# Performance work log

Measured on AMD Instinct MI355X. Metric: run time of the kernel, lower is better.

## Reference

```python
import jax, jax.numpy as jnp
import numpy as np

# Graph sizes: each graph has exactly 32 nodes (forced by the rearrange + lin1 in_features)
BS = 4096
NODES = 32
N = BS * NODES          # 131072 total nodes
F_IN = 128
E_PER_G = 512
E = BS * E_PER_G        # 2097152 edges, all within-graph
HID = 1024
NCLS = 10


def setup_inputs() -> dict:
    key = jax.random.key(0)
    ks = jax.random.split(key, 9)
    x = jax.random.normal(ks[0], (N, F_IN), dtype=jnp.float32)
    # within-graph random edges: local node ids in [0,32) + per-graph offset
    graph_off = jnp.repeat(jnp.arange(BS, dtype=jnp.int64), E_PER_G) * NODES
    src = jax.random.randint(ks[1], (E,), 0, NODES, dtype=jnp.int64) + graph_off
    dst = jax.random.randint(ks[2], (E,), 0, NODES, dtype=jnp.int64) + graph_off
    edge_index = jnp.stack([src, dst], axis=0)
    s = 0.05
    gconv_w = jax.random.normal(ks[3], (F_IN, F_IN), dtype=jnp.float32) * s
    gconv_b = jax.random.normal(ks[4], (F_IN,), dtype=jnp.float32) * s
    lin1_w = jax.random.normal(ks[5], (HID, F_IN * NODES), dtype=jnp.float32) * s
    lin1_b = jax.random.normal(ks[6], (HID,), dtype=jnp.float32) * s
    lin2_w = jax.random.normal(ks[7], (NCLS, HID), dtype=jnp.float32) * s
    lin2_b = jax.random.normal(ks[8], (NCLS,), dtype=jnp.float32) * s
    return {"x": x, "edge_index": edge_index, "gconv_w": gconv_w,
            "gconv_b": gconv_b, "lin1_w": lin1_w, "lin1_b": lin1_b,
            "lin2_w": lin2_w, "lin2_b": lin2_b, "bs": BS}


def reference(x, edge_index, gconv_w, gconv_b, lin1_w, lin1_b, lin2_w, lin2_b, bs):
    # GINConv (eps=0): h_i = Linear( x_i + sum_{j->i} x_j )
    src, dst = edge_index[0], edge_index[1]
    agg = jax.ops.segment_sum(x[src], dst, num_segments=x.shape[0])  # [N, F]
    h = (x + agg) @ gconv_w.T + gconv_b                               # [N, F]
    h = jax.nn.relu(h)
    # rearrange '(bs e) f -> bs (f e)' with e=32 nodes per graph
    f = h.shape[-1]
    h = h.reshape(bs, NODES, f).transpose(0, 2, 1).reshape(bs, f * NODES)
    h = h @ lin1_w.T + lin1_b
    # dropout is identity in eval mode
    h = jax.nn.relu(h)
    h = h @ lin2_w.T + lin2_b
    return jax.nn.softmax(h, axis=-1)
```

## Files before the change

kernel.cpp:

```cpp
#include <hip/hip_runtime.h>

typedef _Float16 half_t;
typedef _Float16 halfv8 __attribute__((ext_vector_type(8)));
typedef _Float16 halfv4 __attribute__((ext_vector_type(4)));
typedef float    floatv4 __attribute__((ext_vector_type(4)));
typedef unsigned int uint;
typedef uint uintv4 __attribute__((ext_vector_type(4)));

#define NODES 32
#define FIN   128
#define EPG   512
#define NBS   4096
#define ETOT  (NBS*EPG)
#define HID   1024
#define KDIM  4096
#define NCLS  10
#define WPITCH 136
#define YPITCH 36

#define GLDS16(g, l)                                                        \
  __builtin_amdgcn_global_load_lds(                                         \
      (const __attribute__((address_space(1))) unsigned int*)(g),           \
      (__attribute__((address_space(3))) unsigned int*)(l), 16, 0, 0)

__global__ __launch_bounds__(256) void prep_w1(const float* __restrict__ w1,
                                               half_t* __restrict__ w1p) {
  __shared__ float tmp[FIN * 33];
  const int o = blockIdx.x, t = threadIdx.x;
  const floatv4* src = (const floatv4*)(w1 + (size_t)o * KDIM);
  for (int i = t; i < KDIM / 4; i += 256) {
    floatv4 v = src[i];
    const int f = i >> 3;
    const int n = (i & 7) * 4;
#pragma unroll
    for (int q = 0; q < 4; ++q) tmp[f * 33 + n + q] = v[q];
  }
  __syncthreads();
  half_t* dst = w1p + (size_t)o * KDIM;
  for (int i = t; i < KDIM; i += 256) {
    const int n = i >> 7, f = i & 127;
    dst[i] = (half_t)tmp[f * 33 + n];
  }
}

__global__ __launch_bounds__(256, 2) void gin_fused(
    const float* __restrict__ x, const int* __restrict__ ei,
    const float* __restrict__ gw, const float* __restrict__ gb,
    half_t* __restrict__ H) {
  __shared__ __attribute__((aligned(16))) half_t Ws[FIN * WPITCH];
  __shared__ __attribute__((aligned(16))) half_t Yt[4][FIN * YPITCH];
  __shared__ __attribute__((aligned(16))) uint  cnt[4][512];

  const int t = threadIdx.x, w = t >> 6, l = t & 63;
  const int lr = l & 15, lk = l >> 4;
  const int g = blockIdx.x * 4 + w;

  const float* xg = x + (size_t)g * (NODES * FIN);
  floatv4 xr[2][4][2];
#pragma unroll
  for (int mt = 0; mt < 2; ++mt)
#pragma unroll
    for (int kk = 0; kk < 4; ++kk) {
      const float* p = xg + (mt * 16 + lr) * FIN + kk * 32 + lk * 8;
      xr[mt][kk][0] = *(const floatv4*)p;
      xr[mt][kk][1] = *(const floatv4*)(p + 4);
    }
  const int* sp = ei + (size_t)g * EPG;
  const int* dp = ei + (size_t)ETOT + (size_t)g * EPG;
  uintv4 s0 = *(const uintv4*)(sp + l * 8);
  uintv4 s1 = *(const uintv4*)(sp + l * 8 + 4);
  uintv4 d0 = *(const uintv4*)(dp + l * 8);
  uintv4 d1 = *(const uintv4*)(dp + l * 8 + 4);

  {
    uintv4* c4 = (uintv4*)cnt[w];
    uintv4 z = {0, 0, 0, 0};
    c4[l] = z;
    c4[l + 64] = z;
  }
  for (int i = t; i < (FIN * FIN) / 4; i += 256) {
    const int o = i >> 5, kc = (i & 31) * 4;
    floatv4 v = *(const floatv4*)(gw + o * FIN + kc);
    halfv4 h = {(half_t)v[0], (half_t)v[1], (half_t)v[2], (half_t)v[3]};
    *(halfv4*)&Ws[o * WPITCH + kc] = h;
  }
  __syncthreads();

#pragma unroll
  for (int q = 0; q < 4; ++q) {
    uint p0 = (d0[q] & 31) * 32 + (s0[q] & 31);
    atomicAdd(&cnt[w][p0 >> 1], 1u << ((p0 & 1) * 16));
    uint p1 = (d1[q] & 31) * 32 + (s1[q] & 31);
    atomicAdd(&cnt[w][p1 >> 1], 1u << ((p1 & 1) * 16));
  }

  halfv8 af[2][4];
#pragma unroll
  for (int mt = 0; mt < 2; ++mt)
#pragma unroll
    for (int kk = 0; kk < 4; ++kk) {
      halfv8 h;
#pragma unroll
      for (int q = 0; q < 4; ++q) {
        h[q]     = (half_t)xr[mt][kk][0][q];
        h[q + 4] = (half_t)xr[mt][kk][1][q];
      }
      af[mt][kk] = h;
    }

  floatv4 acc[2][8] = {};
#pragma unroll
  for (int kk = 0; kk < 4; ++kk)
#pragma unroll
    for (int nt = 0; nt < 8; ++nt) {
      halfv8 bf = *(const halfv8*)&Ws[(nt * 16 + lr) * WPITCH + kk * 32 + lk * 8];
#pragma unroll
      for (int mt = 0; mt < 2; ++mt)
        acc[mt][nt] = __builtin_amdgcn_mfma_f32_16x16x32_f16(af[mt][kk], bf,
                                                             acc[mt][nt], 0, 0, 0);
    }

  half_t* yw = Yt[w];
#pragma unroll
  for (int mt = 0; mt < 2; ++mt)
#pragma unroll
    for (int nt = 0; nt < 8; ++nt) {
      halfv4 h = {(half_t)acc[mt][nt][0], (half_t)acc[mt][nt][1],
                  (half_t)acc[mt][nt][2], (half_t)acc[mt][nt][3]};
      *(halfv4*)&yw[(nt * 16 + lr) * YPITCH + mt * 16 + lk * 4] = h;
    }

  const unsigned short* c16 = (const unsigned short*)cnt[w];
  halfv8 am[2];
#pragma unroll
  for (int mt = 0; mt < 2; ++mt) {
    const int i = mt * 16 + lr;
#pragma unroll
    for (int q = 0; q < 8; ++q) {
      const int j = lk * 8 + q;
      float c = (float)c16[i * 32 + j] + ((j == i) ? 1.f : 0.f);
      am[mt][q] = (half_t)c;
    }
  }

  floatv4 acc2[2][8] = {};
#pragma unroll
  for (int nt = 0; nt < 8; ++nt) {
    halfv8 bf = *(const halfv8*)&yw[(nt * 16 + lr) * YPITCH + lk * 8];
#pragma unroll
    for (int mt = 0; mt < 2; ++mt)
      acc2[mt][nt] = __builtin_amdgcn_mfma_f32_16x16x32_f16(am[mt], bf,
                                                            acc2[mt][nt], 0, 0, 0);
  }

  half_t* Hg = H + (size_t)g * KDIM;
#pragma unroll
  for (int nt = 0; nt < 8; ++nt) {
    const float bias = gb[nt * 16 + lr];
#pragma unroll
    for (int mt = 0; mt < 2; ++mt)
#pragma unroll
      for (int q = 0; q < 4; ++q) {
        const int m = mt * 16 + lk * 4 + q;
        const float v = acc2[mt][nt][q] + bias;
        Hg[m * FIN + nt * 16 + lr] = (half_t)(v > 0.f ? v : 0.f);
      }
  }
}

__global__ __launch_bounds__(256) void lin1_gemm(
    const half_t* __restrict__ A, const half_t* __restrict__ B,
    half_t* __restrict__ Cbase) {
  __shared__ __attribute__((aligned(16))) half_t As[128 * 32];
  __shared__ __attribute__((aligned(16))) half_t Bs[128 * 32];
  const int t = threadIdx.x;
  const int m0 = blockIdx.x * 128;
  const int n0 = blockIdx.y * 128;
  const int kz = blockIdx.z;
  const int k0 = kz * (KDIM / 2);
  half_t* C = Cbase + (size_t)kz * ((size_t)NBS * HID);

  const int w = t >> 6, l = t & 63;
  const int lr = l & 15, lk = l >> 4;
  const int wm = (w & 1) * 64, wn = (w >> 1) * 64;

  const int ch0 = t, ch1 = t + 256;
  const int r0 = ch0 >> 2, c0_ = (ch0 & 3) * 8;
  const int r1 = ch1 >> 2, c1_ = (ch1 & 3) * 8;
  const half_t* gA0 = A + (size_t)(m0 + r0) * KDIM + k0 + c0_;
  const half_t* gA1 = A + (size_t)(m0 + r1) * KDIM + k0 + c1_;
  const half_t* gB0 = B + (size_t)(n0 + r0) * KDIM + k0 + c0_;
  const half_t* gB1 = B + (size_t)(n0 + r1) * KDIM + k0 + c1_;

  floatv4 acc[4][4] = {};

  for (int kt = 0; kt < 64; ++kt) {
    GLDS16(gA0, &As[ch0 * 8]);
    GLDS16(gA1, &As[ch1 * 8]);
    GLDS16(gB0, &Bs[ch0 * 8]);
    GLDS16(gB1, &Bs[ch1 * 8]);
    gA0 += 32; gA1 += 32; gB0 += 32; gB1 += 32;
    __syncthreads();

    halfv8 af[4], bf[4];
#pragma unroll
    for (int mf = 0; mf < 4; ++mf)
      af[mf] = *(const halfv8*)&As[(wm + mf * 16 + lr) * 32 + lk * 8];
#pragma unroll
    for (int nf = 0; nf < 4; ++nf)
      bf[nf] = *(const halfv8*)&Bs[(wn + nf * 16 + lr) * 32 + lk * 8];
#pragma unroll
    for (int mf = 0; mf < 4; ++mf)
#pragma unroll
      for (int nf = 0; nf < 4; ++nf)
        acc[mf][nf] = __builtin_amdgcn_mfma_f32_16x16x32_f16(af[mf], bf[nf],
                                                             acc[mf][nf], 0, 0, 0);
    __syncthreads();
  }
#pragma unroll
  for (int mf = 0; mf < 4; ++mf)
#pragma unroll
    for (int nf = 0; nf < 4; ++nf) {
      const int n = n0 + wn + nf * 16 + lr;
#pragma unroll
      for (int j = 0; j < 4; ++j) {
        const int m = m0 + wm + mf * 16 + lk * 4 + j;
        C[(size_t)m * HID + n] = (half_t)acc[mf][nf][j];
      }
    }
}

__global__ __launch_bounds__(256) void head(
    const half_t* __restrict__ C0, const half_t* __restrict__ C1,
    const float* __restrict__ b1, const float* __restrict__ w2,
    const float* __restrict__ b2, float* __restrict__ out) {
  __shared__ __attribute__((aligned(16))) float w2s[NCLS * HID];
  const int t = threadIdx.x;
  {
    const floatv4* s4 = (const floatv4*)w2;
    floatv4* d4 = (floatv4*)w2s;
    for (int i = t; i < (NCLS * HID) / 4; i += 256) d4[i] = s4[i];
  }
  __syncthreads();
  const int w = t >> 6, l = t & 63;
  const int row = blockIdx.x * 4 + w;
  const half_t* c0 = C0 + (size_t)row * HID;
  const half_t* c1 = C1 + (size_t)row * HID;

  float r[16];
#pragma unroll
  for (int jj = 0; jj < 4; ++jj) {
    halfv4 u = *(const halfv4*)&c0[jj * 256 + l * 4];
    halfv4 v = *(const halfv4*)&c1[jj * 256 + l * 4];
    floatv4 bb = *(const floatv4*)&b1[jj * 256 + l * 4];
#pragma unroll
    for (int q = 0; q < 4; ++q) {
      const float s = (float)u[q] + (float)v[q] + bb[q];
      r[jj * 4 + q] = s > 0.f ? s : 0.f;
    }
  }
  float lg[10];
#pragma unroll
  for (int c = 0; c < NCLS; ++c) {
    float p = 0.f;
#pragma unroll
    for (int jj = 0; jj < 4; ++jj) {
      floatv4 wv = *(const floatv4*)&w2s[c * HID + jj * 256 + l * 4];
      p += r[jj * 4 + 0] * wv[0] + r[jj * 4 + 1] * wv[1] +
           r[jj * 4 + 2] * wv[2] + r[jj * 4 + 3] * wv[3];
    }
#pragma unroll
    for (int off = 32; off >= 1; off >>= 1) p += __shfl_xor(p, off);
    lg[c] = p + b2[c];
  }
  float mx = lg[0];
#pragma unroll
  for (int c = 1; c < NCLS; ++c) mx = fmaxf(mx, lg[c]);
  float sum = 0.f;
#pragma unroll
  for (int c = 0; c < NCLS; ++c) { lg[c] = __expf(lg[c] - mx); sum += lg[c]; }
  const float inv = 1.f / sum;
  float myv = 0.f;
#pragma unroll
  for (int c = 0; c < NCLS; ++c) myv = (l == c) ? lg[c] * inv : myv;
  if (l < NCLS) out[(size_t)row * NCLS + l] = myv;
}

extern "C" void kernel_launch(void* const* d_in, const int* in_sizes, int n_in,
                              void* d_out, int out_size, void* d_ws, size_t ws_size,
                              hipStream_t stream) {
  (void)in_sizes; (void)n_in; (void)out_size; (void)ws_size;
  const float* x  = (const float*)d_in[0];
  const int*   ei = (const int*)d_in[1];
  const float* gw = (const float*)d_in[2];
  const float* gb = (const float*)d_in[3];
  const float* w1 = (const float*)d_in[4];
  const float* b1 = (const float*)d_in[5];
  const float* w2 = (const float*)d_in[6];
  const float* b2 = (const float*)d_in[7];
  float* out = (float*)d_out;

  char* ws = (char*)d_ws;
  half_t* H   = (half_t*)(ws);
  half_t* w1p = (half_t*)(ws + 33554432);
  half_t* C01 = (half_t*)(ws + 33554432 + 8388608);

  prep_w1  <<<dim3(HID),       dim3(256), 0, stream>>>(w1, w1p);
  gin_fused<<<dim3(NBS / 4),   dim3(256), 0, stream>>>(x, ei, gw, gb, H);
  lin1_gemm<<<dim3(32, 8, 2),  dim3(256), 0, stream>>>(H, w1p, C01);
  head     <<<dim3(NBS / 4),   dim3(256), 0, stream>>>(C01, C01 + (size_t)NBS * HID,
                                                       b1, w2, b2, out);
}
```

Measured before the change: 100.3 us.

## Rewrite lin1 GEMM with 256x256 tiles, double-buffered swizzled LDS, 4-way split-K

Replaces the 128x128x32 single-buffered lin1 GEMM with 512-thread blocks computing 256x256 tiles and BK=64. Global-to-LDS loads are double-buffered, LDS chunks are XOR-swizzled to avoid bank conflicts, and MFMA bursts are bracketed with setprio. The block index is remapped to group tiles, and K is split four ways, so the head kernel now sums four fp16 partials. This aims to cut global traffic per flop and hide load latency. The costs are more partial-sum traffic and LDS pressure: 128KB per block with launch_bounds(512,2).

```diff
diff --git a/kernel.cpp b/kernel.cpp
--- a/kernel.cpp
+++ b/kernel.cpp
@@ -18,6 +18,13 @@
 #define WPITCH 136
 #define YPITCH 36
 
+#define BM 256
+#define BN 256
+#define BK 64
+#define KS 4
+#define KSLEN (KDIM/KS)
+#define NT (KSLEN/BK)
+
 #define GLDS16(g, l)                                                        \
   __builtin_amdgcn_global_load_lds(                                         \
       (const __attribute__((address_space(1))) unsigned int*)(g),           \
@@ -168,72 +175,125 @@
   }
 }
 
-__global__ __launch_bounds__(256) void lin1_gemm(
+__global__ __launch_bounds__(512, 2) void lin1_gemm(
     const half_t* __restrict__ A, const half_t* __restrict__ B,
     half_t* __restrict__ Cbase) {
-  __shared__ __attribute__((aligned(16))) half_t As[128 * 32];
-  __shared__ __attribute__((aligned(16))) half_t Bs[128 * 32];
+  __shared__ __attribute__((aligned(16))) half_t As[2][BM * BK];
+  __shared__ __attribute__((aligned(16))) half_t Bs[2][BN * BK];
+
   const int t = threadIdx.x;
-  const int m0 = blockIdx.x * 128;
-  const int n0 = blockIdx.y * 128;
-  const int kz = blockIdx.z;
-  const int k0 = kz * (KDIM / 2);
-  half_t* C = Cbase + (size_t)kz * ((size_t)NBS * HID);
-
-  const int w = t >> 6, l = t & 63;
-  const int lr = l & 15, lk = l >> 4;
-  const int wm = (w & 1) * 64, wn = (w >> 1) * 64;
-
-  const int ch0 = t, ch1 = t + 256;
-  const int r0 = ch0 >> 2, c0_ = (ch0 & 3) * 8;
-  const int r1 = ch1 >> 2, c1_ = (ch1 & 3) * 8;
-  const half_t* gA0 = A + (size_t)(m0 + r0) * KDIM + k0 + c0_;
-  const half_t* gA1 = A + (size_t)(m0 + r1) * KDIM + k0 + c1_;
-  const half_t* gB0 = B + (size_t)(n0 + r0) * KDIM + k0 + c0_;
-  const half_t* gB1 = B + (size_t)(n0 + r1) * KDIM + k0 + c1_;
-
-  floatv4 acc[4][4] = {};
-
-  for (int kt = 0; kt < 64; ++kt) {
-    GLDS16(gA0, &As[ch0 * 8]);
-    GLDS16(gA1, &As[ch1 * 8]);
-    GLDS16(gB0, &Bs[ch0 * 8]);
-    GLDS16(gB1, &Bs[ch1 * 8]);
-    gA0 += 32; gA1 += 32; gB0 += 32; gB1 += 32;
-    __syncthreads();
-
-    halfv8 af[4], bf[4];
-#pragma unroll
-    for (int mf = 0; mf < 4; ++mf)
-      af[mf] = *(const halfv8*)&As[(wm + mf * 16 + lr) * 32 + lk * 8];
-#pragma unroll
-    for (int nf = 0; nf < 4; ++nf)
-      bf[nf] = *(const halfv8*)&Bs[(wn + nf * 16 + lr) * 32 + lk * 8];
-#pragma unroll
-    for (int mf = 0; mf < 4; ++mf)
-#pragma unroll
-      for (int nf = 0; nf < 4; ++nf)
-        acc[mf][nf] = __builtin_amdgcn_mfma_f32_16x16x32_f16(af[mf], bf[nf],
-                                                             acc[mf][nf], 0, 0, 0);
-    __syncthreads();
-  }
-#pragma unroll
-  for (int mf = 0; mf < 4; ++mf)
+  const int orig = blockIdx.x;
+  const int wg = (orig & 7) * 32 + (orig >> 3);
+  const int mt = wg & 15, rest = wg >> 4;
+  const int nt_ = rest & 3, ks = rest >> 2;
+  const int m0 = mt * BM, n0 = nt_ * BN, k0 = ks * KSLEN;
+
+  const half_t* gA[4];
+  const half_t* gB[4];
+#pragma unroll
+  for (int j = 0; j < 4; ++j) {
+    const int L = t + j * 512;
+    const int r = L >> 3;
+    const int c = (L & 7) ^ (r & 7);
+    gA[j] = A + (size_t)(m0 + r) * KDIM + k0 + c * 8;
+    gB[j] = B + (size_t)(n0 + r) * KDIM + k0 + c * 8;
+  }
+
+#define STAGE(buf, koff)                                                    \
+  {                                                                         \
+    _Pragma("unroll")                                                       \
+    for (int j = 0; j < 4; ++j)                                             \
+      GLDS16(gA[j] + (koff), &As[buf][(t + j * 512) * 8]);                  \
+    _Pragma("unroll")                                                       \
+    for (int j = 0; j < 4; ++j)                                             \
+      GLDS16(gB[j] + (koff), &Bs[buf][(t + j * 512) * 8]);                  \
+  }
+
+  const int w = t >> 6, l = t & 63, lr = l & 15, lk = l >> 4;
+  const int wm = (w >> 2) * 128, wn = (w & 3) * 64;
+
+  floatv4 acc[8][4] = {};
+
+  STAGE(0, 0)
+  STAGE(1, BK)
+  asm volatile("s_waitcnt vmcnt(8)" ::: "memory");
+  __builtin_amdgcn_s_barrier();
+
+  for (int kt = 0; kt < NT; ++kt) {
+    const int cur = kt & 1;
+    const half_t* as = As[cur];
+    const half_t* bs = Bs[cur];
+    halfv8 bf[4], af[4];
+#pragma unroll
+    for (int ksb = 0; ksb < 2; ++ksb) {
+#pragma unroll
+      for (int nf = 0; nf < 4; ++nf) {
+        const int row = wn + nf * 16 + lr;
+        const int ch = (ksb * 4 + lk) ^ (row & 7);
+        bf[nf] = *(const halfv8*)&bs[row * BK + ch * 8];
+      }
+#pragma unroll
+      for (int mf = 0; mf < 4; ++mf) {
+        const int row = wm + mf * 16 + lr;
+        const int ch = (ksb * 4 + lk) ^ (row & 7);
+        af[mf] = *(const halfv8*)&as[row * BK + ch * 8];
+      }
+      __builtin_amdgcn_s_barrier();
+      asm volatile("s_waitcnt lgkmcnt(0)" ::: "memory");
+      __builtin_amdgcn_sched_barrier(0);
+      __builtin_amdgcn_s_setprio(1);
+#pragma unroll
+      for (int mf = 0; mf < 4; ++mf)
+#pragma unroll
+        for (int nf = 0; nf < 4; ++nf)
+          acc[mf][nf] = __builtin_amdgcn_mfma_f32_16x16x32_f16(
+              af[mf], bf[nf], acc[mf][nf], 0, 0, 0);
+      __builtin_amdgcn_s_setprio(0);
+      __builtin_amdgcn_s_barrier();
+#pragma unroll
+      for (int mf = 0; mf < 4; ++mf) {
+        const int row = wm + 64 + mf * 16 + lr;
+        const int ch = (ksb * 4 + lk) ^ (row & 7);
+        af[mf] = *(const halfv8*)&as[row * BK + ch * 8];
+      }
+      __builtin_amdgcn_s_barrier();
+      asm volatile("s_waitcnt lgkmcnt(0)" ::: "memory");
+      __builtin_amdgcn_sched_barrier(0);
+      __builtin_amdgcn_s_setprio(1);
+#pragma unroll
+      for (int mf = 0; mf < 4; ++mf)
+#pragma unroll
+        for (int nf = 0; nf < 4; ++nf)
+          acc[mf + 4][nf] = __builtin_amdgcn_mfma_f32_16x16x32_f16(
+              af[mf], bf[nf], acc[mf + 4][nf], 0, 0, 0);
+      __builtin_amdgcn_s_setprio(0);
+      __builtin_amdgcn_s_barrier();
+    }
+    const int src = (kt + 2 < NT) ? (kt + 2) : 0;
+    STAGE(cur, src * BK)
+    asm volatile("s_waitcnt vmcnt(8)" ::: "memory");
+    __builtin_amdgcn_s_barrier();
+  }
+
+  half_t* C = Cbase + (size_t)ks * ((size_t)NBS * HID);
+#pragma unroll
+  for (int mf = 0; mf < 8; ++mf)
 #pragma unroll
     for (int nf = 0; nf < 4; ++nf) {
       const int n = n0 + wn + nf * 16 + lr;
 #pragma unroll
-      for (int j = 0; j < 4; ++j) {
-        const int m = m0 + wm + mf * 16 + lk * 4 + j;
-        C[(size_t)m * HID + n] = (half_t)acc[mf][nf][j];
-      }
-    }
+      for (int q = 0; q < 4; ++q) {
+        const int m = m0 + wm + mf * 16 + lk * 4 + q;
+        C[(size_t)m * HID + n] = (half_t)acc[mf][nf][q];
+      }
+    }
+#undef STAGE
 }
 
 __global__ __launch_bounds__(256) void head(
-    const half_t* __restrict__ C0, const half_t* __restrict__ C1,
-    const float* __restrict__ b1, const float* __restrict__ w2,
-    const float* __restrict__ b2, float* __restrict__ out) {
+    const half_t* __restrict__ Cb, const float* __restrict__ b1,
+    const float* __restrict__ w2, const float* __restrict__ b2,
+    float* __restrict__ out) {
   __shared__ __attribute__((aligned(16))) float w2s[NCLS * HID];
   const int t = threadIdx.x;
   {
@@ -244,20 +304,21 @@
   __syncthreads();
   const int w = t >> 6, l = t & 63;
   const int row = blockIdx.x * 4 + w;
-  const half_t* c0 = C0 + (size_t)row * HID;
-  const half_t* c1 = C1 + (size_t)row * HID;
 
   float r[16];
 #pragma unroll
   for (int jj = 0; jj < 4; ++jj) {
-    halfv4 u = *(const halfv4*)&c0[jj * 256 + l * 4];
-    halfv4 v = *(const halfv4*)&c1[jj * 256 + l * 4];
     floatv4 bb = *(const floatv4*)&b1[jj * 256 + l * 4];
-#pragma unroll
-    for (int q = 0; q < 4; ++q) {
-      const float s = (float)u[q] + (float)v[q] + bb[q];
-      r[jj * 4 + q] = s > 0.f ? s : 0.f;
-    }
+    float s[4] = {bb[0], bb[1], bb[2], bb[3]};
+#pragma unroll
+    for (int p = 0; p < KS; ++p) {
+      const half_t* cp = Cb + (size_t)p * ((size_t)NBS * HID) + (size_t)row * HID;
+      halfv4 u = *(const halfv4*)&cp[jj * 256 + l * 4];
+#pragma unroll
+      for (int q = 0; q < 4; ++q) s[q] += (float)u[q];
+    }
+#pragma unroll
+    for (int q = 0; q < 4; ++q) r[jj * 4 + q] = s[q] > 0.f ? s[q] : 0.f;
   }
   float lg[10];
 #pragma unroll
@@ -303,11 +364,10 @@
   char* ws = (char*)d_ws;
   half_t* H   = (half_t*)(ws);
   half_t* w1p = (half_t*)(ws + 33554432);
-  half_t* C01 = (half_t*)(ws + 33554432 + 8388608);
-
-  prep_w1  <<<dim3(HID),       dim3(256), 0, stream>>>(w1, w1p);
-  gin_fused<<<dim3(NBS / 4),   dim3(256), 0, stream>>>(x, ei, gw, gb, H);
-  lin1_gemm<<<dim3(32, 8, 2),  dim3(256), 0, stream>>>(H, w1p, C01);
-  head     <<<dim3(NBS / 4),   dim3(256), 0, stream>>>(C01, C01 + (size_t)NBS * HID,
-                                                       b1, w2, b2, out);
-}
+  half_t* C   = (half_t*)(ws + 33554432 + 8388608);
+
+  prep_w1  <<<dim3(HID),     dim3(256), 0, stream>>>(w1, w1p);
+  gin_fused<<<dim3(NBS / 4), dim3(256), 0, stream>>>(x, ei, gw, gb, H);
+  lin1_gemm<<<dim3(16 * 4 * KS), dim3(512), 0, stream>>>(H, w1p, C);
+  head     <<<dim3(NBS / 4), dim3(256), 0, stream>>>(C, b1, w2, b2, out);
+}
```

Measured after the change: 98.62 us. No clear change (-1.7%).
